# Kernel optimization log

Measured on AMD Instinct MI355X. Metric: run time of the kernel, lower is better.

The kernel has to match this reference:

```python
import jax, jax.numpy as jnp
import numpy as np

N_NODES = 50000
N_EDGES = 800000
IN_DIM, HID_DIM, OUT_DIM = 64, 128, 32


def _mpnn_layer(x, src, dst, W, b):
    # message: linear on gathered source features (x_j), then mean-scatter to dst
    msg = x[src] @ W + b                      # [E, out]
    agg = jax.ops.segment_sum(msg, dst, num_segments=N_NODES)
    deg = jax.ops.segment_sum(jnp.ones((msg.shape[0],), msg.dtype), dst,
                              num_segments=N_NODES)
    return agg / jnp.maximum(deg, 1.0)[:, None]  # mean; isolated nodes -> 0


def setup_inputs() -> dict:
    key = jax.random.key(0)
    ks = jax.random.split(key, 8)
    x = jax.random.normal(ks[0], (N_NODES, IN_DIM), dtype=jnp.float32)
    edge_index = jax.random.randint(ks[1], (2, N_EDGES), 0, N_NODES, dtype=jnp.int64)
    W1 = jax.random.normal(ks[2], (IN_DIM, HID_DIM), dtype=jnp.float32) * 0.1
    b1 = jax.random.normal(ks[3], (HID_DIM,), dtype=jnp.float32) * 0.1
    W2 = jax.random.normal(ks[4], (HID_DIM, HID_DIM), dtype=jnp.float32) * 0.1
    b2 = jax.random.normal(ks[5], (HID_DIM,), dtype=jnp.float32) * 0.1
    Wout = jax.random.normal(ks[6], (HID_DIM, OUT_DIM), dtype=jnp.float32) * 0.1
    bout = jax.random.normal(ks[7], (OUT_DIM,), dtype=jnp.float32) * 0.1
    return {"x": x, "edge_index": edge_index, "W1": W1, "b1": b1,
            "W2": W2, "b2": b2, "Wout": Wout, "bout": bout}


def reference(x, edge_index, W1, b1, W2, b2, Wout, bout):
    src, dst = edge_index[0], edge_index[1]  # PyG flow: source_to_target
    h = jax.nn.relu(_mpnn_layer(x, src, dst, W1, b1))
    h = jax.nn.relu(_mpnn_layer(h, src, dst, W2, b2))
    return h @ Wout + bout
```

## Files before the change

kernel.cpp:

```cpp
#include <hip/hip_runtime.h>
#include <hip/hip_bf16.h>

#define N_NODES 50000
#define N_EDGES 800000
#define IN_DIM  64
#define HID_DIM 128
#define OUT_DIM 32
#define ELLW    64

#define NRANGE   8
#define RNG      (N_NODES / NRANGE)
#define ELL_BLKS 25000

#define CAST_BLKS 3125
#define PW1_BLKS  32
#define PW2_BLKS  64
#define PWO_BLKS  16
#define PREP_BLKS (CAST_BLKS + PW1_BLKS + PW2_BLKS + PWO_BLKS)

typedef short bh8_t  __attribute__((ext_vector_type(8)));
typedef float fx4_t  __attribute__((ext_vector_type(4)));

__device__ inline float bflo(unsigned int u) {
    union { unsigned int i; float f; } c; c.i = u << 16; return c.f;
}
__device__ inline float bfhi(unsigned int u) {
    union { unsigned int i; float f; } c; c.i = u & 0xffff0000u; return c.f;
}
__device__ inline unsigned short f2bf(float f) {
    union { float f; unsigned int i; } c; c.f = f;
    unsigned int u = c.i;
    u += 0x7fffu + ((u >> 16) & 1u);
    return (unsigned short)(u >> 16);
}
__device__ inline unsigned int pack2(float a, float b) {
    return (unsigned int)f2bf(a) | ((unsigned int)f2bf(b) << 16);
}
__device__ inline void acc_u2(float* a, uint2 u) {
    a[0] += bflo(u.x); a[1] += bfhi(u.x);
    a[2] += bflo(u.y); a[3] += bfhi(u.y);
}
__device__ inline void acc_u4(float* a, uint4 u) {
    a[0] += bflo(u.x); a[1] += bfhi(u.x);
    a[2] += bflo(u.y); a[3] += bfhi(u.y);
    a[4] += bflo(u.z); a[5] += bfhi(u.z);
    a[6] += bflo(u.w); a[7] += bfhi(u.w);
}

template <int K, int M>
__device__ inline void packw_one(const float* __restrict__ W,
                                 unsigned short* __restrict__ Wp, int f) {
    const int k = f / M, m = f % M;
    Wp[((k >> 3) * M + m) * 8 + (k & 7)] = f2bf(W[f]);
}

__global__ __launch_bounds__(256) void k_pe(const int* __restrict__ src,
                                            const int* __restrict__ dst,
                                            int* __restrict__ cnt,
                                            int* __restrict__ ell,
                                            const float* __restrict__ x,
                                            unsigned short* __restrict__ xb,
                                            const float* __restrict__ W1,
                                            unsigned short* __restrict__ wp1,
                                            const float* __restrict__ W2,
                                            unsigned short* __restrict__ wp2,
                                            const float* __restrict__ Wout,
                                            unsigned short* __restrict__ wpo) {
    const int bid = blockIdx.x;
    if (bid < ELL_BLKS) {
        const int r  = bid & (NRANGE - 1);
        const int j  = bid >> 3;
        const int lo = r * RNG;
        const int e  = j * 256 + threadIdx.x;
        const int d  = dst[e];
        if ((unsigned)(d - lo) < (unsigned)RNG) {
            const int p = atomicAdd(&cnt[d], 1);
            if (p < ELLW) ell[(size_t)d * ELLW + p] = src[e];
        }
        return;
    }
    const int pb = bid - ELL_BLKS;
    if (pb < CAST_BLKS) {
        const int i = pb * 256 + threadIdx.x;
        float4 v = reinterpret_cast<const float4*>(x)[i];
        ushort4 o;
        o.x = f2bf(v.x); o.y = f2bf(v.y); o.z = f2bf(v.z); o.w = f2bf(v.w);
        reinterpret_cast<ushort4*>(xb)[i] = o;
    } else if (pb < CAST_BLKS + PW1_BLKS) {
        packw_one<IN_DIM, HID_DIM>(W1, wp1, (pb - CAST_BLKS) * 256 + threadIdx.x);
    } else if (pb < CAST_BLKS + PW1_BLKS + PW2_BLKS) {
        packw_one<HID_DIM, HID_DIM>(W2, wp2, (pb - CAST_BLKS - PW1_BLKS) * 256 + threadIdx.x);
    } else {
        packw_one<HID_DIM, OUT_DIM>(Wout, wpo,
                                    (pb - CAST_BLKS - PW1_BLKS - PW2_BLKS) * 256 + threadIdx.x);
    }
}

__global__ __launch_bounds__(256) void k_agg1(const unsigned short* __restrict__ Xb,
                                              const int* __restrict__ ell,
                                              const int* __restrict__ cnt,
                                              unsigned short* __restrict__ Mb) {
    const int gid  = threadIdx.x >> 4;
    const int lane = threadIdx.x & 15;
    const int node = blockIdx.x * 16 + gid;
    const int c = min(cnt[node], ELLW);
    const float r = (c > 0) ? 1.0f / (float)c : 0.0f;
    const int* er = ell + (size_t)node * ELLW;
    const unsigned short* base = Xb + lane * 4;

    float a0[4], a1[4];
#pragma unroll
    for (int v = 0; v < 4; ++v) { a0[v] = 0.f; a1[v] = 0.f; }

    int j = 0;
    for (; j + 8 <= c; j += 8) {
        const int4 e03 = *reinterpret_cast<const int4*>(er + j);
        const int4 e47 = *reinterpret_cast<const int4*>(er + j + 4);
        uint2 u0 = *reinterpret_cast<const uint2*>(base + (size_t)e03.x * IN_DIM);
        uint2 u1 = *reinterpret_cast<const uint2*>(base + (size_t)e03.y * IN_DIM);
        uint2 u2 = *reinterpret_cast<const uint2*>(base + (size_t)e03.z * IN_DIM);
        uint2 u3 = *reinterpret_cast<const uint2*>(base + (size_t)e03.w * IN_DIM);
        uint2 u4 = *reinterpret_cast<const uint2*>(base + (size_t)e47.x * IN_DIM);
        uint2 u5 = *reinterpret_cast<const uint2*>(base + (size_t)e47.y * IN_DIM);
        uint2 u6 = *reinterpret_cast<const uint2*>(base + (size_t)e47.z * IN_DIM);
        uint2 u7 = *reinterpret_cast<const uint2*>(base + (size_t)e47.w * IN_DIM);
        acc_u2(a0, u0); acc_u2(a1, u1); acc_u2(a0, u2); acc_u2(a1, u3);
        acc_u2(a0, u4); acc_u2(a1, u5); acc_u2(a0, u6); acc_u2(a1, u7);
    }
    for (; j + 4 <= c; j += 4) {
        const int4 e4 = *reinterpret_cast<const int4*>(er + j);
        uint2 u0 = *reinterpret_cast<const uint2*>(base + (size_t)e4.x * IN_DIM);
        uint2 u1 = *reinterpret_cast<const uint2*>(base + (size_t)e4.y * IN_DIM);
        uint2 u2 = *reinterpret_cast<const uint2*>(base + (size_t)e4.z * IN_DIM);
        uint2 u3 = *reinterpret_cast<const uint2*>(base + (size_t)e4.w * IN_DIM);
        acc_u2(a0, u0); acc_u2(a1, u1); acc_u2(a0, u2); acc_u2(a1, u3);
    }
    for (; j < c; ++j) {
        uint2 u = *reinterpret_cast<const uint2*>(base + (size_t)er[j] * IN_DIM);
        acc_u2(a0, u);
    }

    uint2 o;
    o.x = pack2((a0[0] + a1[0]) * r, (a0[1] + a1[1]) * r);
    o.y = pack2((a0[2] + a1[2]) * r, (a0[3] + a1[3]) * r);
    *reinterpret_cast<uint2*>(Mb + (size_t)node * IN_DIM + lane * 4) = o;
}

__global__ __launch_bounds__(256) void k_mgemm1(const unsigned short* __restrict__ A,
                                                const unsigned short* __restrict__ Wpg,
                                                const float* __restrict__ b1,
                                                const int* __restrict__ cnt,
                                                unsigned short* __restrict__ h1b) {
    __shared__ unsigned short Wp[IN_DIM * HID_DIM];
    const int tid = threadIdx.x;
#pragma unroll
    for (int f = tid; f < IN_DIM * HID_DIM / 8; f += 256)
        reinterpret_cast<uint4*>(Wp)[f] = reinterpret_cast<const uint4*>(Wpg)[f];
    __syncthreads();

    const int w  = tid >> 6;
    const int l  = tid & 63;
    const int lr = l & 15;
    const int lg = l >> 4;
    const int row = blockIdx.x * 64 + w * 16 + lr;
    const bool rok = row < N_NODES;
    const unsigned short* Arow = A + (size_t)row * IN_DIM;

    fx4_t acc[8];
#pragma unroll
    for (int ct = 0; ct < 8; ++ct) acc[ct] = (fx4_t){0.f, 0.f, 0.f, 0.f};

#pragma unroll
    for (int kc = 0; kc < IN_DIM; kc += 32) {
        bh8_t af = {};
        if (rok) af = *reinterpret_cast<const bh8_t*>(Arow + kc + lg * 8);
#pragma unroll
        for (int ct = 0; ct < 8; ++ct) {
            const bh8_t bf = *reinterpret_cast<const bh8_t*>(
                &Wp[(((kc >> 3) + lg) * HID_DIM + ct * 16 + lr) * 8]);
            acc[ct] = __builtin_amdgcn_mfma_f32_16x16x32_bf16(af, bf, acc[ct], 0, 0, 0);
        }
    }

    const int orow0 = blockIdx.x * 64 + w * 16 + lg * 4;
    bool on[4];
#pragma unroll
    for (int r = 0; r < 4; ++r)
        on[r] = (orow0 + r < N_NODES) && (cnt[orow0 + r] > 0);

#pragma unroll
    for (int ct = 0; ct < 8; ++ct) {
        const int m = ct * 16 + lr;
        const float bm = b1[m];
#pragma unroll
        for (int r = 0; r < 4; ++r) {
            const int n = orow0 + r;
            if (n < N_NODES) {
                float v = on[r] ? fmaxf(acc[ct][r] + bm, 0.f) : 0.f;
                h1b[(size_t)n * HID_DIM + m] = f2bf(v);
            }
        }
    }
}

__global__ __launch_bounds__(256) void k_agg2(const unsigned short* __restrict__ Xb,
                                              const int* __restrict__ ell,
                                              const int* __restrict__ cnt,
                                              unsigned short* __restrict__ Mb) {
    const int gid  = threadIdx.x >> 4;
    const int lane = threadIdx.x & 15;
    const int node = blockIdx.x * 16 + gid;
    const int c = min(cnt[node], ELLW);
    const float r = (c > 0) ? 1.0f / (float)c : 0.0f;
    const int* er = ell + (size_t)node * ELLW;
    const unsigned short* base = Xb + lane * 8;

    float a0[8], a1[8];
#pragma unroll
    for (int v = 0; v < 8; ++v) { a0[v] = 0.f; a1[v] = 0.f; }

    int j = 0;
    for (; j + 8 <= c; j += 8) {
        const int4 e03 = *reinterpret_cast<const int4*>(er + j);
        const int4 e47 = *reinterpret_cast<const int4*>(er + j + 4);
        uint4 u0 = *reinterpret_cast<const uint4*>(base + (size_t)e03.x * HID_DIM);
        uint4 u1 = *reinterpret_cast<const uint4*>(base + (size_t)e03.y * HID_DIM);
        uint4 u2 = *reinterpret_cast<const uint4*>(base + (size_t)e03.z * HID_DIM);
        uint4 u3 = *reinterpret_cast<const uint4*>(base + (size_t)e03.w * HID_DIM);
        uint4 u4 = *reinterpret_cast<const uint4*>(base + (size_t)e47.x * HID_DIM);
        uint4 u5 = *reinterpret_cast<const uint4*>(base + (size_t)e47.y * HID_DIM);
        uint4 u6 = *reinterpret_cast<const uint4*>(base + (size_t)e47.z * HID_DIM);
        uint4 u7 = *reinterpret_cast<const uint4*>(base + (size_t)e47.w * HID_DIM);
        acc_u4(a0, u0); acc_u4(a1, u1); acc_u4(a0, u2); acc_u4(a1, u3);
        acc_u4(a0, u4); acc_u4(a1, u5); acc_u4(a0, u6); acc_u4(a1, u7);
    }
    for (; j + 4 <= c; j += 4) {
        const int4 e4 = *reinterpret_cast<const int4*>(er + j);
        uint4 u0 = *reinterpret_cast<const uint4*>(base + (size_t)e4.x * HID_DIM);
        uint4 u1 = *reinterpret_cast<const uint4*>(base + (size_t)e4.y * HID_DIM);
        uint4 u2 = *reinterpret_cast<const uint4*>(base + (size_t)e4.z * HID_DIM);
        uint4 u3 = *reinterpret_cast<const uint4*>(base + (size_t)e4.w * HID_DIM);
        acc_u4(a0, u0); acc_u4(a1, u1); acc_u4(a0, u2); acc_u4(a1, u3);
    }
    for (; j < c; ++j) {
        uint4 u = *reinterpret_cast<const uint4*>(base + (size_t)er[j] * HID_DIM);
        acc_u4(a0, u);
    }

    uint4 o;
    o.x = pack2((a0[0] + a1[0]) * r, (a0[1] + a1[1]) * r);
    o.y = pack2((a0[2] + a1[2]) * r, (a0[3] + a1[3]) * r);
    o.z = pack2((a0[4] + a1[4]) * r, (a0[5] + a1[5]) * r);
    o.w = pack2((a0[6] + a1[6]) * r, (a0[7] + a1[7]) * r);
    *reinterpret_cast<uint4*>(Mb + (size_t)node * HID_DIM + lane * 8) = o;
}

#define H2S (HID_DIM + 8)
__global__ __launch_bounds__(256) void k_mgemm23(const unsigned short* __restrict__ A,
                                                 const unsigned short* __restrict__ Wp2g,
                                                 const unsigned short* __restrict__ Wpog,
                                                 const float* __restrict__ b2,
                                                 const float* __restrict__ bout,
                                                 const int* __restrict__ cnt,
                                                 float* __restrict__ out) {
    __shared__ unsigned short Wp2s[HID_DIM * HID_DIM];
    __shared__ unsigned short Wpos[HID_DIM * OUT_DIM];
    __shared__ unsigned short h2s[64 * H2S];
    const int tid = threadIdx.x;
#pragma unroll
    for (int f = tid; f < HID_DIM * HID_DIM / 8; f += 256)
        reinterpret_cast<uint4*>(Wp2s)[f] = reinterpret_cast<const uint4*>(Wp2g)[f];
#pragma unroll
    for (int f = tid; f < HID_DIM * OUT_DIM / 8; f += 256)
        reinterpret_cast<uint4*>(Wpos)[f] = reinterpret_cast<const uint4*>(Wpog)[f];
    __syncthreads();

    const int w  = tid >> 6;
    const int l  = tid & 63;
    const int lr = l & 15;
    const int lg = l >> 4;
    const int row = blockIdx.x * 64 + w * 16 + lr;
    const bool rok = row < N_NODES;
    const unsigned short* Arow = A + (size_t)row * HID_DIM;

    fx4_t acc[8];
#pragma unroll
    for (int ct = 0; ct < 8; ++ct) acc[ct] = (fx4_t){0.f, 0.f, 0.f, 0.f};

#pragma unroll
    for (int kc = 0; kc < HID_DIM; kc += 32) {
        bh8_t af = {};
        if (rok) af = *reinterpret_cast<const bh8_t*>(Arow + kc + lg * 8);
#pragma unroll
        for (int ct = 0; ct < 8; ++ct) {
            const bh8_t bf = *reinterpret_cast<const bh8_t*>(
                &Wp2s[(((kc >> 3) + lg) * HID_DIM + ct * 16 + lr) * 8]);
            acc[ct] = __builtin_amdgcn_mfma_f32_16x16x32_bf16(af, bf, acc[ct], 0, 0, 0);
        }
    }

    const int lrow0 = w * 16 + lg * 4;
    const int orow0 = blockIdx.x * 64 + lrow0;
    bool on[4];
#pragma unroll
    for (int r = 0; r < 4; ++r)
        on[r] = (orow0 + r < N_NODES) && (cnt[orow0 + r] > 0);

#pragma unroll
    for (int ct = 0; ct < 8; ++ct) {
        const int m = ct * 16 + lr;
        const float bm = b2[m];
#pragma unroll
        for (int r = 0; r < 4; ++r) {
            float v = on[r] ? fmaxf(acc[ct][r] + bm, 0.f) : 0.f;
            h2s[(lrow0 + r) * H2S + m] = f2bf(v);
        }
    }
    __syncthreads();

    fx4_t acc2[2];
#pragma unroll
    for (int ct = 0; ct < 2; ++ct) acc2[ct] = (fx4_t){0.f, 0.f, 0.f, 0.f};

#pragma unroll
    for (int kc = 0; kc < HID_DIM; kc += 32) {
        const bh8_t af = *reinterpret_cast<const bh8_t*>(
            &h2s[(w * 16 + lr) * H2S + kc + lg * 8]);
#pragma unroll
        for (int ct = 0; ct < 2; ++ct) {
            const bh8_t bf = *reinterpret_cast<const bh8_t*>(
                &Wpos[(((kc >> 3) + lg) * OUT_DIM + ct * 16 + lr) * 8]);
            acc2[ct] = __builtin_amdgcn_mfma_f32_16x16x32_bf16(af, bf, acc2[ct], 0, 0, 0);
        }
    }

#pragma unroll
    for (int ct = 0; ct < 2; ++ct) {
        const int m = ct * 16 + lr;
        const float bm = bout[m];
#pragma unroll
        for (int r = 0; r < 4; ++r) {
            const int n = orow0 + r;
            if (n < N_NODES)
                out[(size_t)n * OUT_DIM + m] = acc2[ct][r] + bm;
        }
    }
}

extern "C" void kernel_launch(void* const* d_in, const int* in_sizes, int n_in,
                              void* d_out, int out_size, void* d_ws, size_t ws_size,
                              hipStream_t stream) {
    const float* x    = (const float*)d_in[0];
    const int*   ei   = (const int*)d_in[1];
    const float* W1   = (const float*)d_in[2];
    const float* b1   = (const float*)d_in[3];
    const float* W2   = (const float*)d_in[4];
    const float* b2   = (const float*)d_in[5];
    const float* Wout = (const float*)d_in[6];
    const float* bout = (const float*)d_in[7];
    float* out = (float*)d_out;

    const int* src = ei;
    const int* dst = ei + N_EDGES;

    char* ws = (char*)d_ws;
    int*            cnt = (int*)(ws + 0);
    int*            ell = (int*)(ws + 200000);
    unsigned short* xb  = (unsigned short*)(ws + 13000000);
    unsigned short* h1b = (unsigned short*)(ws + 19400000);
    unsigned short* m2b = (unsigned short*)(ws + 32200000);
    unsigned short* m1b = (unsigned short*)(ws + 45000000);
    unsigned short* wp1 = (unsigned short*)(ws + 51400000);
    unsigned short* wp2 = (unsigned short*)(ws + 51416384);
    unsigned short* wpo = (unsigned short*)(ws + 51449152);

    const int GB = (N_NODES + 63) / 64;
    const int AB = N_NODES / 16;

    hipMemsetAsync(cnt, 0, N_NODES * sizeof(int), stream);

    k_pe<<<ELL_BLKS + PREP_BLKS, 256, 0, stream>>>(src, dst, cnt, ell,
                                                   x, xb, W1, wp1, W2, wp2, Wout, wpo);

    k_agg1<<<AB, 256, 0, stream>>>(xb, ell, cnt, m1b);
    k_mgemm1<<<GB, 256, 0, stream>>>(m1b, wp1, b1, cnt, h1b);

    k_agg2<<<AB, 256, 0, stream>>>(h1b, ell, cnt, m2b);

    k_mgemm23<<<GB, 256, 0, stream>>>(m2b, wp2, wpo, b2, bout, cnt, out);
}
```

Before: 131.9 us.

## Shard per-node edge counters to cut atomic contention, then compact into ELL

Edge bucketing no longer has eight range-filtered passes that each read all edges. It now does one pass with counters sharded by block (8 per node), writing into a 128-slot-per-node staging buffer. A new compaction kernel prefix-sums the shard counts and packs the entries into the original 64-wide ELL layout plus a total count. This removes the redundant reads of dst and spreads atomic contention across shards. The cost is an extra kernel launch, a larger memset and staging buffer, and a 16-per-shard overflow cap that can drop edges on skewed degrees.

```diff
diff --git a/kernel.cpp b/kernel.cpp
--- a/kernel.cpp
+++ b/kernel.cpp
@@ -7,11 +7,10 @@
 #define HID_DIM 128
 #define OUT_DIM 32
 #define ELLW    64
-
-#define NRANGE   8
-#define RNG      (N_NODES / NRANGE)
-#define ELL_BLKS 25000
-
+#define NSHARD  8
+#define SSLOT   16
+
+#define SC_BLKS  3125
 #define CAST_BLKS 3125
 #define PW1_BLKS  32
 #define PW2_BLKS  64
@@ -56,8 +55,8 @@
 
 __global__ __launch_bounds__(256) void k_pe(const int* __restrict__ src,
                                             const int* __restrict__ dst,
-                                            int* __restrict__ cnt,
-                                            int* __restrict__ ell,
+                                            int* __restrict__ cnt8,
+                                            int* __restrict__ ell2,
                                             const float* __restrict__ x,
                                             unsigned short* __restrict__ xb,
                                             const float* __restrict__ W1,
@@ -67,19 +66,16 @@
                                             const float* __restrict__ Wout,
                                             unsigned short* __restrict__ wpo) {
     const int bid = blockIdx.x;
-    if (bid < ELL_BLKS) {
-        const int r  = bid & (NRANGE - 1);
-        const int j  = bid >> 3;
-        const int lo = r * RNG;
-        const int e  = j * 256 + threadIdx.x;
-        const int d  = dst[e];
-        if ((unsigned)(d - lo) < (unsigned)RNG) {
-            const int p = atomicAdd(&cnt[d], 1);
-            if (p < ELLW) ell[(size_t)d * ELLW + p] = src[e];
-        }
+    if (bid < SC_BLKS) {
+        const int shard = bid & (NSHARD - 1);
+        const int e = bid * 256 + threadIdx.x;
+        const int d = dst[e];
+        const int p = atomicAdd(&cnt8[d * NSHARD + shard], 1);
+        if (p < SSLOT)
+            ell2[(size_t)d * (NSHARD * SSLOT) + shard * SSLOT + p] = src[e];
         return;
     }
-    const int pb = bid - ELL_BLKS;
+    const int pb = bid - SC_BLKS;
     if (pb < CAST_BLKS) {
         const int i = pb * 256 + threadIdx.x;
         float4 v = reinterpret_cast<const float4*>(x)[i];
@@ -94,6 +90,35 @@
         packw_one<HID_DIM, OUT_DIM>(Wout, wpo,
                                     (pb - CAST_BLKS - PW1_BLKS - PW2_BLKS) * 256 + threadIdx.x);
     }
+}
+
+__global__ __launch_bounds__(256) void k_cmp(const int* __restrict__ ell2,
+                                             const int* __restrict__ cnt8,
+                                             int* __restrict__ ell,
+                                             int* __restrict__ cnt) {
+    const int wid  = threadIdx.x >> 6;
+    const int lane = threadIdx.x & 63;
+    const int node = blockIdx.x * 4 + wid;
+    int cs = 0;
+    if (lane < NSHARD) cs = min(cnt8[node * NSHARD + lane], SSLOT);
+    int total = 0, pre = 0;
+#pragma unroll
+    for (int s = 0; s < NSHARD; ++s) {
+        const int t = __shfl(cs, s, 64);
+        total += t;
+        if (s < lane) pre += t;
+    }
+#pragma unroll
+    for (int k = 0; k < 2; ++k) {
+        const int slot  = lane + k * 64;
+        const int shard = slot >> 4, j = slot & (SSLOT - 1);
+        const int c_s = __shfl(cs, shard, 64);
+        const int p_s = __shfl(pre, shard, 64);
+        if (j < c_s)
+            ell[(size_t)node * ELLW + p_s + j] =
+                ell2[(size_t)node * (NSHARD * SSLOT) + slot];
+    }
+    if (lane == 0) cnt[node] = total;
 }
 
 __global__ __launch_bounds__(256) void k_agg1(const unsigned short* __restrict__ Xb,
@@ -364,23 +389,28 @@
     const int* dst = ei + N_EDGES;
 
     char* ws = (char*)d_ws;
-    int*            cnt = (int*)(ws + 0);
-    int*            ell = (int*)(ws + 200000);
-    unsigned short* xb  = (unsigned short*)(ws + 13000000);
-    unsigned short* h1b = (unsigned short*)(ws + 19400000);
-    unsigned short* m2b = (unsigned short*)(ws + 32200000);
-    unsigned short* m1b = (unsigned short*)(ws + 45000000);
-    unsigned short* wp1 = (unsigned short*)(ws + 51400000);
-    unsigned short* wp2 = (unsigned short*)(ws + 51416384);
-    unsigned short* wpo = (unsigned short*)(ws + 51449152);
+    int*            cnt8 = (int*)(ws + 0);
+    int*            ell2 = (int*)(ws + 1600000);
+    int*            ell  = (int*)(ws + 27200000);
+    int*            cnt  = (int*)(ws + 40000000);
+    unsigned short* xb   = (unsigned short*)(ws + 40200000);
+    unsigned short* h1b  = (unsigned short*)(ws + 46600000);
+    unsigned short* m2b  = (unsigned short*)(ws + 59400000);
+    unsigned short* m1b  = (unsigned short*)(ws + 72200000);
+    unsigned short* wp1  = (unsigned short*)(ws + 78600000);
+    unsigned short* wp2  = (unsigned short*)(ws + 78616384);
+    unsigned short* wpo  = (unsigned short*)(ws + 78649152);
 
     const int GB = (N_NODES + 63) / 64;
     const int AB = N_NODES / 16;
-
-    hipMemsetAsync(cnt, 0, N_NODES * sizeof(int), stream);
-
-    k_pe<<<ELL_BLKS + PREP_BLKS, 256, 0, stream>>>(src, dst, cnt, ell,
-                                                   x, xb, W1, wp1, W2, wp2, Wout, wpo);
+    const int CB = N_NODES / 4;
+
+    hipMemsetAsync(cnt8, 0, N_NODES * NSHARD * sizeof(int), stream);
+
+    k_pe<<<SC_BLKS + PREP_BLKS, 256, 0, stream>>>(src, dst, cnt8, ell2,
+                                                  x, xb, W1, wp1, W2, wp2, Wout, wpo);
+
+    k_cmp<<<CB, 256, 0, stream>>>(ell2, cnt8, ell, cnt);
 
     k_agg1<<<AB, 256, 0, stream>>>(xb, ell, cnt, m1b);
     k_mgemm1<<<GB, 256, 0, stream>>>(m1b, wp1, b1, cnt, h1b);
```

After: 148.2 us. +12.4%, slower.

## Fold counter zeroing into prep kernel and split ELL fill into chunked kernel

Applied to the files above, without the earlier changes.

Replaces the hipMemsetAsync of the degree counters with zeroing blocks inside a new prep kernel that also casts x to bf16 and packs the weights. ELL construction moves to its own kernel, where each block handles a 2048-edge chunk for one destination range instead of one 256-edge tile. This drops one memset launch and cuts the block count for the fill. In exchange the cast/pack work no longer overlaps with the atomic-heavy fill, and there is an extra kernel boundary.

```diff
diff --git a/kernel.cpp b/kernel.cpp
--- a/kernel.cpp
+++ b/kernel.cpp
@@ -10,13 +10,14 @@
 
 #define NRANGE   8
 #define RNG      (N_NODES / NRANGE)
-#define ELL_BLKS 25000
+#define FILL_CH  2048
+#define FILL_NJ  ((N_EDGES + FILL_CH - 1) / FILL_CH)
 
 #define CAST_BLKS 3125
 #define PW1_BLKS  32
 #define PW2_BLKS  64
 #define PWO_BLKS  16
-#define PREP_BLKS (CAST_BLKS + PW1_BLKS + PW2_BLKS + PWO_BLKS)
+#define ZERO_BLKS 49
 
 typedef short bh8_t  __attribute__((ext_vector_type(8)));
 typedef float fx4_t  __attribute__((ext_vector_type(4)));
@@ -54,45 +55,53 @@
     Wp[((k >> 3) * M + m) * 8 + (k & 7)] = f2bf(W[f]);
 }
 
-__global__ __launch_bounds__(256) void k_pe(const int* __restrict__ src,
-                                            const int* __restrict__ dst,
-                                            int* __restrict__ cnt,
-                                            int* __restrict__ ell,
-                                            const float* __restrict__ x,
-                                            unsigned short* __restrict__ xb,
-                                            const float* __restrict__ W1,
-                                            unsigned short* __restrict__ wp1,
-                                            const float* __restrict__ W2,
-                                            unsigned short* __restrict__ wp2,
-                                            const float* __restrict__ Wout,
-                                            unsigned short* __restrict__ wpo) {
+__global__ void k_prep(const float* __restrict__ x, unsigned short* __restrict__ xb,
+                       const float* __restrict__ W1, unsigned short* __restrict__ wp1,
+                       const float* __restrict__ W2, unsigned short* __restrict__ wp2,
+                       const float* __restrict__ Wout, unsigned short* __restrict__ wpo,
+                       int* __restrict__ cnt) {
     const int bid = blockIdx.x;
-    if (bid < ELL_BLKS) {
-        const int r  = bid & (NRANGE - 1);
-        const int j  = bid >> 3;
-        const int lo = r * RNG;
-        const int e  = j * 256 + threadIdx.x;
-        const int d  = dst[e];
-        if ((unsigned)(d - lo) < (unsigned)RNG) {
-            const int p = atomicAdd(&cnt[d], 1);
-            if (p < ELLW) ell[(size_t)d * ELLW + p] = src[e];
-        }
-        return;
-    }
-    const int pb = bid - ELL_BLKS;
-    if (pb < CAST_BLKS) {
-        const int i = pb * 256 + threadIdx.x;
+    if (bid < CAST_BLKS) {
+        const int i = bid * 256 + threadIdx.x;
         float4 v = reinterpret_cast<const float4*>(x)[i];
         ushort4 o;
         o.x = f2bf(v.x); o.y = f2bf(v.y); o.z = f2bf(v.z); o.w = f2bf(v.w);
         reinterpret_cast<ushort4*>(xb)[i] = o;
-    } else if (pb < CAST_BLKS + PW1_BLKS) {
-        packw_one<IN_DIM, HID_DIM>(W1, wp1, (pb - CAST_BLKS) * 256 + threadIdx.x);
-    } else if (pb < CAST_BLKS + PW1_BLKS + PW2_BLKS) {
-        packw_one<HID_DIM, HID_DIM>(W2, wp2, (pb - CAST_BLKS - PW1_BLKS) * 256 + threadIdx.x);
+    } else if (bid < CAST_BLKS + PW1_BLKS) {
+        packw_one<IN_DIM, HID_DIM>(W1, wp1, (bid - CAST_BLKS) * 256 + threadIdx.x);
+    } else if (bid < CAST_BLKS + PW1_BLKS + PW2_BLKS) {
+        packw_one<HID_DIM, HID_DIM>(W2, wp2, (bid - CAST_BLKS - PW1_BLKS) * 256 + threadIdx.x);
+    } else if (bid < CAST_BLKS + PW1_BLKS + PW2_BLKS + PWO_BLKS) {
+        packw_one<HID_DIM, OUT_DIM>(Wout, wpo,
+                                    (bid - CAST_BLKS - PW1_BLKS - PW2_BLKS) * 256 + threadIdx.x);
     } else {
-        packw_one<HID_DIM, OUT_DIM>(Wout, wpo,
-                                    (pb - CAST_BLKS - PW1_BLKS - PW2_BLKS) * 256 + threadIdx.x);
+        const int zb = bid - (CAST_BLKS + PW1_BLKS + PW2_BLKS + PWO_BLKS);
+#pragma unroll
+        for (int k2 = 0; k2 < 4; ++k2) {
+            const int i = zb * 1024 + k2 * 256 + threadIdx.x;
+            if (i < N_NODES) cnt[i] = 0;
+        }
+    }
+}
+
+__global__ __launch_bounds__(256) void k_ell(const int* __restrict__ src,
+                                             const int* __restrict__ dst,
+                                             int* __restrict__ cnt,
+                                             int* __restrict__ ell) {
+    const int r    = blockIdx.x & (NRANGE - 1);
+    const int j    = blockIdx.x >> 3;
+    const int lo   = r * RNG;
+    const int base = j * FILL_CH;
+#pragma unroll
+    for (int i = 0; i < FILL_CH / 256; ++i) {
+        const int e = base + i * 256 + threadIdx.x;
+        if (e < N_EDGES) {
+            const int d = dst[e];
+            if ((unsigned)(d - lo) < (unsigned)RNG) {
+                const int p = atomicAdd(&cnt[d], 1);
+                if (p < ELLW) ell[(size_t)d * ELLW + p] = src[e];
+            }
+        }
     }
 }
 
@@ -377,10 +386,10 @@
     const int GB = (N_NODES + 63) / 64;
     const int AB = N_NODES / 16;
 
-    hipMemsetAsync(cnt, 0, N_NODES * sizeof(int), stream);
-
-    k_pe<<<ELL_BLKS + PREP_BLKS, 256, 0, stream>>>(src, dst, cnt, ell,
-                                                   x, xb, W1, wp1, W2, wp2, Wout, wpo);
+    k_prep<<<CAST_BLKS + PW1_BLKS + PW2_BLKS + PWO_BLKS + ZERO_BLKS, 256, 0, stream>>>(
+        x, xb, W1, wp1, W2, wp2, Wout, wpo, cnt);
+
+    k_ell<<<FILL_NJ * NRANGE, 256, 0, stream>>>(src, dst, cnt, ell);
 
     k_agg1<<<AB, 256, 0, stream>>>(xb, ell, cnt, m1b);
     k_mgemm1<<<GB, 256, 0, stream>>>(m1b, wp1, b1, cnt, h1b);
```

Result: no change. 131.0 us (median of 2 runs) (-0.6%).
